# Kernel optimization log

Measured on AMD Instinct MI355X. Metric: run time of the kernel, lower is better.

## Reference

```python
import jax, jax.numpy as jnp
import numpy as np

N, E = 16384, 65536
N2, A2, E2 = 65536, 131072, 262144
N3, A3, E3 = 65536, 196608, 262144
B = 256
F_IN, NI2, NI3 = 16, 64, 64


def setup_inputs() -> dict:
    key = jax.random.key(0)
    ks = iter(jax.random.split(key, 80))
    def rn(shape, s=1.0):
        return jax.random.normal(next(ks), shape, jnp.float32) * s
    def ru(shape):
        return jax.random.uniform(next(ks), shape, dtype=jnp.float32)
    def ri(shape, hi):
        return jax.random.randint(next(ks), shape, 0, hi)
    s = 0.05
    inp = {
        "x": rn((N, F_IN)),
        "edge_index": ri((2, E), N),
        "edge_attr": ru((E, 7)),
        "batch": jnp.sort(ri((N,), B)),
        "assign2_node": ri((A2,), N),
        "assign2_cluster": ri((A2,), N2),
        "iso_type_2": ru((N2, NI2)),
        "edge_index_2": ri((2, E2), N2),
        "batch_2": jnp.sort(ri((N2,), B)),
        "assign3_node": ri((A3,), N),
        "assign3_cluster": ri((A3,), N3),
        "iso_type_3": ru((N3, NI3)),
        "edge_index_3": ri((2, E3), N3),
        "batch_3": jnp.sort(ri((N3,), B)),
    }
    for i, (mi, mo) in enumerate([(F_IN, 32), (32, 64), (64, 64)], start=1):
        inp[f"nn{i}_W1"] = rn((7, 128), s)
        inp[f"nn{i}_b1"] = jnp.zeros((128,), jnp.float32)
        inp[f"nn{i}_W2"] = rn((128, mi * mo), s)
        inp[f"nn{i}_b2"] = jnp.zeros((mi * mo,), jnp.float32)
        inp[f"conv{i}_root"] = rn((mi, mo), s)
        inp[f"conv{i}_bias"] = jnp.zeros((mo,), jnp.float32)
    for i, din in zip([4, 5, 6, 7], [64 + NI2, 64, 64 + NI3, 64]):
        inp[f"conv{i}_Wrel"] = rn((din, 64), s)
        inp[f"conv{i}_Wroot"] = rn((din, 64), s)
        inp[f"conv{i}_bias"] = jnp.zeros((64,), jnp.float32)
    inp["fc1_W"] = rn((384, 64), s); inp["fc1_b"] = jnp.zeros((64,), jnp.float32)
    inp["fc2_W"] = rn((64, 32), s); inp["fc2_b"] = jnp.zeros((32,), jnp.float32)
    inp["fc3_W"] = rn((32, 1), s); inp["fc3_b"] = jnp.zeros((1,), jnp.float32)
    return inp


def nnconv(x, ei, ea, W1, b1, W2, b2, root, bias, mi, mo):
    # edge MLP -> per-edge [mi, mo] weight matrix; message = x_src @ W_e; scatter-add to dst
    h = jax.nn.relu(ea @ W1 + b1) @ W2 + b2          # [E, mi*mo]
    We = h.reshape(-1, mi, mo)
    msg = jnp.einsum('ei,eio->eo', x[ei[0]], We)     # [E, mo]
    agg = jax.ops.segment_sum(msg, ei[1], num_segments=x.shape[0])
    return x @ root + agg + bias


def graphconv(x, ei, Wrel, Wroot, bias):
    agg = jax.ops.segment_sum(x[ei[0]], ei[1], num_segments=x.shape[0])
    return agg @ Wrel + x @ Wroot + bias


def avg_pool_assign(x, node_idx, cluster_idx, num_clusters):
    s = jax.ops.segment_sum(x[node_idx], cluster_idx, num_segments=num_clusters)
    c = jax.ops.segment_sum(jnp.ones((node_idx.shape[0],), x.dtype), cluster_idx, num_segments=num_clusters)
    return s / jnp.clip(c, 1.0)[:, None]


def reference(x, edge_index, edge_attr, batch, assign2_node, assign2_cluster, iso_type_2, edge_index_2, batch_2, assign3_node, assign3_cluster, iso_type_3, edge_index_3, batch_3, nn1_W1, nn1_b1, nn1_W2, nn1_b2, conv1_root, conv1_bias, nn2_W1, nn2_b1, nn2_W2, nn2_b2, conv2_root, conv2_bias, nn3_W1, nn3_b1, nn3_W2, nn3_b2, conv3_root, conv3_bias, conv4_Wrel, conv4_Wroot, conv4_bias, conv5_Wrel, conv5_Wroot, conv5_bias, conv6_Wrel, conv6_Wroot, conv6_bias, conv7_Wrel, conv7_Wroot, conv7_bias, fc1_W, fc1_b, fc2_W, fc2_b, fc3_W, fc3_b):
    elu = jax.nn.elu
    h = elu(nnconv(x, edge_index, edge_attr, nn1_W1, nn1_b1, nn1_W2, nn1_b2, conv1_root, conv1_bias, F_IN, 32))
    h = elu(nnconv(h, edge_index, edge_attr, nn2_W1, nn2_b1, nn2_W2, nn2_b2, conv2_root, conv2_bias, 32, 64))
    h = elu(nnconv(h, edge_index, edge_attr, nn3_W1, nn3_b1, nn3_W2, nn3_b2, conv3_root, conv3_bias, 64, 64))
    x_1 = jax.ops.segment_sum(h, batch, num_segments=B)
    # 2-set level
    h2 = avg_pool_assign(h, assign2_node, assign2_cluster, N2)
    h2 = jnp.concatenate([h2, iso_type_2], axis=1)
    h2 = elu(graphconv(h2, edge_index_2, conv4_Wrel, conv4_Wroot, conv4_bias))
    h2 = elu(graphconv(h2, edge_index_2, conv5_Wrel, conv5_Wroot, conv5_bias))
    x_2 = jax.ops.segment_sum(h2, batch_2, num_segments=B)
    # 3-set level
    h3 = avg_pool_assign(h, assign3_node, assign3_cluster, N3)
    h3 = jnp.concatenate([h3, iso_type_3], axis=1)
    h3 = elu(graphconv(h3, edge_index_3, conv6_Wrel, conv6_Wroot, conv6_bias))
    h3 = elu(graphconv(h3, edge_index_3, conv7_Wrel, conv7_Wroot, conv7_bias))
    x_3 = jax.ops.segment_sum(h3, batch_3, num_segments=B)
    xc = jnp.concatenate([x_1, x_2, x_3], axis=1)
    xc = jnp.concatenate([xc, xc], axis=1)      # [B, 384]
    o = elu(xc @ fc1_W + fc1_b)
    o = elu(o @ fc2_W + fc2_b)
    o = o @ fc3_W + fc3_b
    return o.reshape(-1)
```

## Files before the change

kernel.cpp:

```cpp
#include <hip/hip_runtime.h>
#include <math.h>

#define NN 16384
#define E1N 65536
#define NBATCH 256
#define NC2 65536
#define KH 128
#define MNSTR 1092
#define OCS 136
#define ECAP 96

typedef _Float16 f16;
typedef _Float16 f16x2 __attribute__((ext_vector_type(2)));
typedef _Float16 f16x4 __attribute__((ext_vector_type(4)));
typedef _Float16 f16x8 __attribute__((ext_vector_type(8)));
typedef float    f32x4 __attribute__((ext_vector_type(4)));

__device__ __forceinline__ float elu1(float x){ return x > 0.f ? x : expm1f(x); }

__device__ __forceinline__ float dot2acc(f16x2 a, f16x2 b, float c){
#if __has_builtin(__builtin_amdgcn_fdot2)
  return __builtin_amdgcn_fdot2(a, b, c, false);
#else
  return fmaf((float)a[0], (float)b[0], fmaf((float)a[1], (float)b[1], c));
#endif
}

__global__ __launch_bounds__(256) void k_count(const int* __restrict__ arr, int* __restrict__ cnt, int n){
  int i = blockIdx.x*256 + threadIdx.x;
  if (i < n) atomicAdd(&cnt[arr[i]], 1);
}

__global__ __launch_bounds__(256) void k_scan1(const int* __restrict__ deg,
    int* __restrict__ ptr, int* __restrict__ partials){
  __shared__ int buf[256];
  int i = blockIdx.x*256 + threadIdx.x, t = threadIdx.x;
  int v = deg[i];
  buf[t] = v; __syncthreads();
  for (int o = 1; o < 256; o <<= 1){
    int x = (t >= o) ? buf[t-o] : 0;
    __syncthreads(); buf[t] += x; __syncthreads();
  }
  ptr[i] = buf[t] - v;
  if (t == 255) partials[blockIdx.x] = buf[255];
}

__global__ __launch_bounds__(256) void k_scan2(int* __restrict__ partials, int nb){
  __shared__ int buf[256];
  int t = threadIdx.x;
  int v = (t < nb) ? partials[t] : 0;
  buf[t] = v; __syncthreads();
  for (int o = 1; o < 256; o <<= 1){
    int x = (t >= o) ? buf[t-o] : 0;
    __syncthreads(); buf[t] += x; __syncthreads();
  }
  if (t < nb) partials[t] = buf[t] - v;
}

__global__ __launch_bounds__(256) void k_scan3(const int* __restrict__ partials,
    int* __restrict__ ptr, int* __restrict__ cur){
  int i = blockIdx.x*256 + threadIdx.x;
  int v = ptr[i] + partials[blockIdx.x];
  ptr[i] = v; cur[i] = v;
}

__global__ __launch_bounds__(256) void k_fill_edge(const int* __restrict__ ei, int* __restrict__ cursor,
    int* __restrict__ eids, int* __restrict__ srcs, int* __restrict__ dsts){
  int e = blockIdx.x*256 + threadIdx.x;
  if (e >= E1N) return;
  int s = ei[e];
  int p = atomicAdd(&cursor[s], 1);
  eids[p] = e; srcs[p] = s; dsts[p] = ei[E1N + e];
}

__global__ __launch_bounds__(256) void k_fill_dst(const int* __restrict__ eiL, int* __restrict__ cur,
    int* __restrict__ dsrc, int EL){
  int e = blockIdx.x*256 + threadIdx.x;
  if (e >= EL) return;
  int d = eiL[EL + e];
  int p = atomicAdd(&cur[d], 1);
  dsrc[p] = eiL[e];
}

__global__ __launch_bounds__(256) void k_fill_assign(const int* __restrict__ an, const int* __restrict__ ac,
    int* __restrict__ cur, int* __restrict__ an_sorted, int A){
  int a = blockIdx.x*256 + threadIdx.x;
  if (a >= A) return;
  int c = ac[a];
  int p = atomicAdd(&cur[c], 1);
  an_sorted[p] = an[a];
}

__global__ __launch_bounds__(256) void k_cvt16(const float* __restrict__ v, f16* __restrict__ o, int n){
  int t = blockIdx.x*256 + threadIdx.x;
  if (t < n) o[t] = (f16)v[t];
}

__global__ __launch_bounds__(256) void k_elu_both(float* __restrict__ v, f16* __restrict__ v16, int n){
  int t = blockIdx.x*256 + threadIdx.x;
  if (t < n){ float r = elu1(v[t]); v[t] = r; v16[t] = (f16)r; }
}

__global__ __launch_bounds__(256) void k_elu(float* __restrict__ v, int n){
  int t = blockIdx.x*256 + threadIdx.x;
  if (t < n) v[t] = elu1(v[t]);
}

__global__ __launch_bounds__(256) void k_packPrep(const float* __restrict__ root,
    const float* __restrict__ b2, f16* __restrict__ Bp, int mi, int mo, int S, int NB){
  int t = blockIdx.x*256 + threadIdx.x;
  if (t >= NB*S*512) return;
  int j = t & 7, l = (t >> 3) & 63, cs = t >> 9;
  int s = cs % S, c = cs / S;
  int k_in = s*32 + ((l>>4)<<3) + j;
  int n = c*16 + (l & 15);
  float v = 0.f;
  if (k_in < mi) v = (n < mo) ? root[k_in*mo + n] : b2[k_in*mo + (n - mo)];
  Bp[t] = (f16)v;
}

template<int MI, int S, int NB, int MO>
__global__ __launch_bounds__(256) void k_prep_mfma(const f16* __restrict__ A,
    const f16* __restrict__ Bp, const float* __restrict__ bias,
    float* __restrict__ outb, float* __restrict__ bterm){
  int l = threadIdx.x & 63, w = threadIdx.x >> 6;
  int r0 = blockIdx.x*64 + w*16;
  const f16* arow = A + (size_t)(r0 + (l & 15))*MI;
  f16x8 a[S];
  #pragma unroll
  for (int s=0;s<S;s++){
    int koff = s*32 + ((l>>4)<<3);
    if (koff < MI) a[s] = *(const f16x8*)(arow + koff);
    else           a[s] = (f16x8){0,0,0,0,0,0,0,0};
  }
  #pragma unroll
  for (int c=0;c<NB;c++){
    f32x4 acc = (f32x4){0.f,0.f,0.f,0.f};
    #pragma unroll
    for (int s=0;s<S;s++){
      f16x8 b = *(const f16x8*)(Bp + ((size_t)(c*S + s)*64 + l)*8);
      acc = __builtin_amdgcn_mfma_f32_16x16x32_f16(a[s], b, acc, 0, 0, 0);
    }
    int col = c*16 + (l & 15);
    #pragma unroll
    for (int r=0;r<4;r++){
      int row = r0 + ((l>>4)<<2) + r;
      if (col < MO) outb[(size_t)row*MO + col] = acc[r] + bias[col];
      else          bterm[(size_t)row*MO + (col - MO)] = acc[r];
    }
  }
}

__global__ __launch_bounds__(256) void k_w2pack_full(const float* __restrict__ W2,
    f16* __restrict__ Bp, int mi, int mo, int S){
  int t = blockIdx.x*256 + threadIdx.x;
  if (t >= mo*8*S*512) return;
  int j = t & 7, l = (t >> 3) & 63, cs = t >> 9;
  int s = cs % S, q = cs / S;
  int oc = q >> 3;
  int k  = (q & 7)*16 + (l & 15);
  int i  = s*32 + ((l>>4)<<3) + j;
  float v = (i < mi) ? W2[(size_t)k*mi*mo + (size_t)i*mo + oc] : 0.f;
  Bp[t] = (f16)v;
}

template<int MI, int S, int MO>
__global__ __launch_bounds__(256) void k_nnconv_fused3(const f16* __restrict__ xin16,
    const f16* __restrict__ W2p,
    const int* __restrict__ rowptr, const int* __restrict__ rowend,
    const int* __restrict__ srcs, const int* __restrict__ dsts,
    const int* __restrict__ eids,
    const float* __restrict__ ea, const float* __restrict__ W1,
    const float* __restrict__ b1,
    const float* __restrict__ bterm, float* __restrict__ outb){
  __shared__ __align__(16) f16   M[16*MNSTR];
  __shared__ __align__(16) f16   hb[ECAP*OCS];
  __shared__ __align__(16) float eas[ECAP*8];
  int t = threadIdx.x, l = t & 63, w = t >> 6;
  int n0 = blockIdx.x*16;
  int estart = rowptr[n0], eend = rowend[n0+15];
  if (estart >= eend) return;
  const f16* arow = xin16 + (size_t)(n0 + (l&15))*MI;
  f16x8 a[S];
  #pragma unroll
  for (int s=0;s<S;s++){
    int koff = s*32 + ((l>>4)<<3);
    if (koff < MI) a[s] = *(const f16x8*)(arow + koff);
    else           a[s] = (f16x8){0,0,0,0,0,0,0,0};
  }
  const int NCHUNK = MO/8;
  int oc = t & 7, eslot = t >> 3;
  for (int ebase = estart; ebase < eend; ebase += ECAP){
    int ecnt = eend - ebase; if (ecnt > ECAP) ecnt = ECAP;
    for (int idx = t; idx < ecnt*8; idx += 256){
      int e_ = idx >> 3, i = idx & 7;
      eas[idx] = (i < 7) ? ea[(size_t)eids[ebase + e_]*7 + i] : 0.f;
    }
    __syncthreads();
    for (int idx = t; idx < ecnt*32; idx += 256){
      int e_ = idx >> 5, p = idx & 31;
      int k0 = p*4;
      const float* xr = &eas[e_*8];
      float4 acc4 = *(const float4*)(b1 + k0);
      #pragma unroll
      for (int i=0;i<7;i++){
        float xv = xr[i];
        float4 wv = *(const float4*)(W1 + i*KH + k0);
        acc4.x = fmaf(xv, wv.x, acc4.x);
        acc4.y = fmaf(xv, wv.y, acc4.y);
        acc4.z = fmaf(xv, wv.z, acc4.z);
        acc4.w = fmaf(xv, wv.w, acc4.w);
      }
      f16x4 hv = { (f16)fmaxf(acc4.x,0.f), (f16)fmaxf(acc4.y,0.f),
                   (f16)fmaxf(acc4.z,0.f), (f16)fmaxf(acc4.w,0.f) };
      *(f16x4*)&hb[e_*OCS + k0] = hv;
    }
    __syncthreads();
    for (int c = 0; c < NCHUNK; c++){
      #pragma unroll
      for (int tt = 0; tt < 16; tt++){
        int q = c*64 + w*16 + tt;
        f32x4 acc = (f32x4){0.f,0.f,0.f,0.f};
        #pragma unroll
        for (int s=0;s<S;s++){
          f16x8 b = *(const f16x8*)(W2p + ((size_t)(q*S + s)*64 + l)*8);
          acc = __builtin_amdgcn_mfma_f32_16x16x32_f16(a[s], b, acc, 0, 0, 0);
        }
        int ocl = w*2 + (tt>>3);
        int kpos = (tt&7)*16 + (l & 15);
        f16* mp = &M[ocl*OCS + kpos];
        #pragma unroll
        for (int r=0;r<4;r++)
          mp[(size_t)(((l>>4)<<2) + r)*MNSTR] = (f16)acc[r];
      }
      __syncthreads();
      #pragma unroll
      for (int r2 = 0; r2 < ECAP/32; r2++){
        int ee = r2*32 + eslot;
        if (ee < ecnt){
          int e = ebase + ee;
          int s_ = srcs[e];
          int ln = s_ - n0;
          float acc = bterm[(size_t)s_*MO + c*8 + oc];
          const f16* mrow = &M[(size_t)ln*MNSTR + oc*OCS];
          const f16* hrow = &hb[ee*OCS];
          #pragma unroll 4
          for (int kk=0; kk<16; kk++){
            f16x8 h8 = *(const f16x8*)(hrow + kk*8);
            f16x4 m0 = *(const f16x4*)(mrow + kk*8);
            f16x4 m1 = *(const f16x4*)(mrow + kk*8 + 4);
            acc = dot2acc((f16x2){h8[0],h8[1]}, (f16x2){m0[0],m0[1]}, acc);
            acc = dot2acc((f16x2){h8[2],h8[3]}, (f16x2){m0[2],m0[3]}, acc);
            acc = dot2acc((f16x2){h8[4],h8[5]}, (f16x2){m1[0],m1[1]}, acc);
            acc = dot2acc((f16x2){h8[6],h8[7]}, (f16x2){m1[2],m1[3]}, acc);
          }
          atomicAdd(&outb[(size_t)dsts[e]*MO + c*8 + oc], acc);
        }
      }
      __syncthreads();
    }
  }
}

__global__ __launch_bounds__(256) void k_pool_gather(const int* __restrict__ aptr,
    const int* __restrict__ aend, const int* __restrict__ an_sorted,
    const float* __restrict__ h, const float* __restrict__ iso,
    f16* __restrict__ h16){
  int l = threadIdx.x & 63, w = threadIdx.x >> 6;
  int c = blockIdx.x*4 + w;
  int st = aptr[c], en = aend[c];
  float acc = 0.f;
  int e = st;
  for (; e+1 < en; e += 2){
    int n0 = an_sorted[e], n1 = an_sorted[e+1];
    acc += h[(size_t)n0*64 + l];
    acc += h[(size_t)n1*64 + l];
  }
  if (e < en) acc += h[(size_t)an_sorted[e]*64 + l];
  int cnt = en - st;
  float val = (cnt > 0) ? acc / (float)cnt : 0.f;
  h16[(size_t)c*128 + l] = (f16)val;
  h16[(size_t)c*128 + 64 + l] = (f16)iso[(size_t)c*64 + l];
}

__global__ __launch_bounds__(256) void k_packB_gc(const float* __restrict__ Wrel,
    const float* __restrict__ Wroot, f16* __restrict__ Bp, int S){
  int t = blockIdx.x*256 + threadIdx.x;
  if (t >= 8*S*512) return;
  int j = t & 7, l = (t >> 3) & 63, cs = t >> 9;
  int s = cs % S, c = cs / S;
  int k = s*32 + ((l>>4)<<3) + j;
  int n = (c<<4) + (l & 15);
  float v = (n < 64) ? Wrel[k*64 + n] : Wroot[k*64 + (n - 64)];
  Bp[t] = (f16)v;
}

template<int S>
__global__ __launch_bounds__(256) void k_gc_mfma(const f16* __restrict__ A,
    const f16* __restrict__ Bp, const float* __restrict__ bias,
    float* __restrict__ y, float* __restrict__ rbuf){
  int l = threadIdx.x & 63, w = threadIdx.x >> 6;
  int r0 = blockIdx.x*64 + w*16;
  const f16* arow = A + (size_t)(r0 + (l & 15))*(S*32);
  f16x8 a[S];
  #pragma unroll
  for (int s=0;s<S;s++) a[s] = *(const f16x8*)(arow + s*32 + ((l>>4)<<3));
  f32x4 acc[8];
  #pragma unroll
  for (int c=0;c<8;c++) acc[c] = (f32x4){0.f,0.f,0.f,0.f};
  #pragma unroll
  for (int c=0;c<8;c++){
    #pragma unroll
    for (int s=0;s<S;s++){
      f16x8 b = *(const f16x8*)(Bp + ((size_t)(c*S + s)*64 + l)*8);
      acc[c] = __builtin_amdgcn_mfma_f32_16x16x32_f16(a[s], b, acc[c], 0, 0, 0);
    }
  }
  #pragma unroll
  for (int c=0;c<8;c++){
    int col = c*16 + (l & 15);
    #pragma unroll
    for (int r=0;r<4;r++){
      int row = r0 + ((l>>4)<<2) + r;
      if (col < 64) y[(size_t)row*64 + col] = acc[c][r];
      else          rbuf[(size_t)row*64 + (col-64)] = acc[c][r] + bias[col-64];
    }
  }
}

template<bool F16OUT>
__global__ __launch_bounds__(256) void k_gc_gather(const int* __restrict__ dptr,
    const int* __restrict__ dend, const int* __restrict__ dsrc,
    const float* __restrict__ y, const float* __restrict__ rbuf,
    f16* __restrict__ o16, float* __restrict__ o32){
  int l = threadIdx.x & 63, w = threadIdx.x >> 6;
  int n = blockIdx.x*4 + w;
  int st = dptr[n], en = dend[n];
  float acc = rbuf[(size_t)n*64 + l];
  int e = st;
  for (; e+1 < en; e += 2){
    int s0 = dsrc[e], s1 = dsrc[e+1];
    acc += y[(size_t)s0*64 + l];
    acc += y[(size_t)s1*64 + l];
  }
  if (e < en) acc += y[(size_t)dsrc[e]*64 + l];
  float r = elu1(acc);
  if (F16OUT) o16[(size_t)n*64 + l] = (f16)r;
  else        o32[(size_t)n*64 + l] = r;
}

__device__ __forceinline__ int lowerb(const int* __restrict__ a, int n, int key){
  int lo = 0, hi = n;
  while (lo < hi){ int m = (lo + hi) >> 1; if (a[m] < key) lo = m + 1; else hi = m; }
  return lo;
}

__global__ __launch_bounds__(256) void k_batchsum_seg(const int* __restrict__ batch,
    const float* __restrict__ h, float* __restrict__ x123, int n_nodes, int off){
  __shared__ float red[4][64];
  int b = blockIdx.x;
  int lo = lowerb(batch, n_nodes, b);
  int hi = lowerb(batch, n_nodes, b+1);
  int col = threadIdx.x & 63, wq = threadIdx.x >> 6;
  float acc = 0.f;
  for (int n = lo + wq; n < hi; n += 4) acc += h[(size_t)n*64 + col];
  red[wq][col] = acc;
  __syncthreads();
  if (threadIdx.x < 64){
    float s = red[0][threadIdx.x] + red[1][threadIdx.x] + red[2][threadIdx.x] + red[3][threadIdx.x];
    x123[b*192 + off + threadIdx.x] = s;
  }
}

__global__ __launch_bounds__(256) void k_fc1(const float* __restrict__ x123,
    const float* __restrict__ W, const float* __restrict__ b, float* __restrict__ t1){
  int t = blockIdx.x*256 + threadIdx.x;
  if (t >= NBATCH*64) return;
  int bb = t >> 6, o = t & 63;
  const float* xr = x123 + bb*192;
  float acc = b[o];
  for (int j=0;j<192;j++) acc = fmaf(xr[j], W[j*64+o] + W[(192+j)*64+o], acc);
  t1[t] = elu1(acc);
}

__global__ __launch_bounds__(256) void k_fc2(const float* __restrict__ t1,
    const float* __restrict__ W, const float* __restrict__ b, float* __restrict__ t2){
  int t = blockIdx.x*256 + threadIdx.x;
  if (t >= NBATCH*32) return;
  int bb = t >> 5, o = t & 31;
  float acc = b[o];
  for (int j=0;j<64;j++) acc = fmaf(t1[bb*64+j], W[j*32+o], acc);
  t2[t] = elu1(acc);
}

__global__ __launch_bounds__(256) void k_fc3(const float* __restrict__ t2,
    const float* __restrict__ W, const float* __restrict__ b, float* __restrict__ out){
  int t = blockIdx.x*256 + threadIdx.x;
  if (t >= NBATCH) return;
  float acc = b[0];
  for (int j=0;j<32;j++) acc = fmaf(t2[t*32+j], W[j], acc);
  out[t] = acc;
}

static inline int cdiv(long long a, int b){ return (int)((a + b - 1) / b); }

extern "C" void kernel_launch(void* const* d_in, const int* in_sizes, int n_in,
                              void* d_out, int out_size, void* d_ws, size_t ws_size,
                              hipStream_t stream) {
  const float* x0    = (const float*)d_in[0];
  const int*   ei    = (const int*)d_in[1];
  const float* ea    = (const float*)d_in[2];
  const int*   batch = (const int*)d_in[3];
  const int*   a2n   = (const int*)d_in[4];
  const int*   a2c   = (const int*)d_in[5];
  const float* iso2  = (const float*)d_in[6];
  const int*   ei2   = (const int*)d_in[7];
  const int*   b2arr = (const int*)d_in[8];
  const int*   a3n   = (const int*)d_in[9];
  const int*   a3c   = (const int*)d_in[10];
  const float* iso3  = (const float*)d_in[11];
  const int*   ei3   = (const int*)d_in[12];
  const int*   b3arr = (const int*)d_in[13];
  const float* nnp[3][6];
  for (int c=0;c<3;c++) for (int p=0;p<6;p++) nnp[c][p] = (const float*)d_in[14 + 6*c + p];
  const float* c4W[3]; const float* c5W[3]; const float* c6W[3]; const float* c7W[3];
  for (int p=0;p<3;p++){ c4W[p]=(const float*)d_in[32+p]; c5W[p]=(const float*)d_in[35+p];
                         c6W[p]=(const float*)d_in[38+p]; c7W[p]=(const float*)d_in[41+p]; }
  const float* fc1W=(const float*)d_in[44]; const float* fc1b=(const float*)d_in[45];
  const float* fc2W=(const float*)d_in[46]; const float* fc2b=(const float*)d_in[47];
  const float* fc3W=(const float*)d_in[48]; const float* fc3b=(const float*)d_in[49];
  float* outp = (float*)d_out;

  char* ws = (char*)d_ws; size_t off = 0;
  auto alloc = [&](size_t bytes)->void*{ void* p = ws + off; off += (bytes + 255) & ~(size_t)255; return p; };
  const size_t SZ_R0 = (size_t)92*1024*1024;
  char* r0 = (char*)alloc(SZ_R0);
  f16*   W2p   = (f16*)r0;
  f16*   prepB = (f16*)(r0 + 2*1024*1024);
  float* bterm = (float*)(r0 + 2*1024*1024 + 64*1024);
  size_t o2 = 0;
  auto a2 = [&](size_t bytes)->char*{ char* p = r0 + o2; o2 += (bytes + 255) & ~(size_t)255; return p; };
  f16*   h16   = (f16*)  a2((size_t)NC2*128*2);
  float* ybuf  = (float*)a2((size_t)NC2*64*4);
  float* rbuf  = (float*)a2((size_t)NC2*64*4);
  float* gB    = (float*)a2((size_t)NC2*64*4);
  f16*   g16   = (f16*)  a2((size_t)NC2*64*2);
  f16*   BpGc  = (f16*)  a2((size_t)8*4*512*2);
  int*   aptr  = (int*)  a2((size_t)NC2*4);
  int*   acur  = (int*)  a2((size_t)NC2*4);
  int*   dptr  = (int*)  a2((size_t)NC2*4);
  int*   dcur  = (int*)  a2((size_t)NC2*4);
  int*   ldeg  = (int*)  a2((size_t)NC2*4);
  int*   ans   = (int*)  a2((size_t)196608*4);
  int*   dsrc  = (int*)  a2((size_t)262144*4);
  float* hA    = (float*)alloc((size_t)NN*32*4);
  float* hB    = (float*)alloc((size_t)NN*64*4);
  float* hC    = (float*)alloc((size_t)NN*64*4);
  f16*   x016  = (f16*)  alloc((size_t)NN*16*2);
  f16*   hA16  = (f16*)  alloc((size_t)NN*32*2);
  f16*   hB16  = (f16*)  alloc((size_t)NN*64*2);
  int*   deg   = (int*)  alloc((size_t)NN*4);
  int*   cursor= (int*)  alloc((size_t)NN*4);
  int*   rowptr= (int*)  alloc((size_t)NN*4);
  int*   eids  = (int*)  alloc((size_t)E1N*4);
  int*   srcs  = (int*)  alloc((size_t)E1N*4);
  int*   dsts  = (int*)  alloc((size_t)E1N*4);
  int*   parts = (int*)  alloc((size_t)256*4);
  float* x123  = (float*)alloc((size_t)NBATCH*192*4);
  float* t1    = (float*)alloc((size_t)NBATCH*64*4);
  float* t2    = (float*)alloc((size_t)NBATCH*32*4);
  (void)ws_size; (void)n_in; (void)in_sizes; (void)out_size;

  auto scan = [&](const int* dg, int n, int* ptr, int* cur){
    k_scan1<<<n/256,256,0,stream>>>(dg, ptr, parts);
    k_scan2<<<1,256,0,stream>>>(parts, n/256);
    k_scan3<<<n/256,256,0,stream>>>(parts, ptr, cur);
  };

  hipMemsetAsync(deg, 0, (size_t)NN*4, stream);
  k_count<<<cdiv(E1N,256),256,0,stream>>>(ei, deg, E1N);
  scan(deg, NN, rowptr, cursor);
  k_fill_edge<<<cdiv(E1N,256),256,0,stream>>>(ei, cursor, eids, srcs, dsts);
  k_cvt16<<<cdiv((long long)NN*16,256),256,0,stream>>>(x0, x016, NN*16);

  auto run_nnconv = [&](const f16* xin16, int mi, int mo,
                        const float* const* P, float* outb, f16* out16){
    const float* W1=P[0]; const float* b1=P[1]; const float* W2=P[2];
    const float* b2=P[3]; const float* root=P[4]; const float* bias=P[5];
    const int S = (mi > 32) ? 2 : 1;
    const int NB = (2*mo)/16;
    k_packPrep<<<cdiv((long long)NB*S*512,256),256,0,stream>>>(root, b2, prepB, mi, mo, S, NB);
    if (mi==16)      k_prep_mfma<16,1,4,32><<<NN/64,256,0,stream>>>(xin16, prepB, bias, outb, bterm);
    else if (mi==32) k_prep_mfma<32,1,8,64><<<NN/64,256,0,stream>>>(xin16, prepB, bias, outb, bterm);
    else             k_prep_mfma<64,2,8,64><<<NN/64,256,0,stream>>>(xin16, prepB, bias, outb, bterm);
    k_w2pack_full<<<cdiv((long long)mo*8*S*512,256),256,0,stream>>>(W2, W2p, mi, mo, S);
    if (mi==16)      k_nnconv_fused3<16,1,32><<<NN/16,256,0,stream>>>(xin16, W2p, rowptr, cursor, srcs, dsts, eids, ea, W1, b1, bterm, outb);
    else if (mi==32) k_nnconv_fused3<32,1,64><<<NN/16,256,0,stream>>>(xin16, W2p, rowptr, cursor, srcs, dsts, eids, ea, W1, b1, bterm, outb);
    else             k_nnconv_fused3<64,2,64><<<NN/16,256,0,stream>>>(xin16, W2p, rowptr, cursor, srcs, dsts, eids, ea, W1, b1, bterm, outb);
    if (out16) k_elu_both<<<cdiv((long long)NN*mo,256),256,0,stream>>>(outb, out16, NN*mo);
    else       k_elu<<<cdiv((long long)NN*mo,256),256,0,stream>>>(outb, NN*mo);
  };
  run_nnconv(x016, 16, 32, nnp[0], hA, hA16);
  run_nnconv(hA16, 32, 64, nnp[1], hB, hB16);
  run_nnconv(hB16, 64, 64, nnp[2], hC, nullptr);

  k_batchsum_seg<<<NBATCH,256,0,stream>>>(batch, hC, x123, NN, 0);

  auto run_level = [&](const int* an, const int* ac, int A, const float* iso,
                       const int* eiL, int EL, const int* batchL,
                       const float* const* cA, const float* const* cB, int off123){
    hipMemsetAsync(ldeg, 0, (size_t)NC2*4, stream);
    k_count<<<cdiv(A,256),256,0,stream>>>(ac, ldeg, A);
    scan(ldeg, NC2, aptr, acur);
    k_fill_assign<<<cdiv(A,256),256,0,stream>>>(an, ac, acur, ans, A);
    hipMemsetAsync(ldeg, 0, (size_t)NC2*4, stream);
    k_count<<<cdiv(EL,256),256,0,stream>>>(eiL + EL, ldeg, EL);
    scan(ldeg, NC2, dptr, dcur);
    k_fill_dst<<<cdiv(EL,256),256,0,stream>>>(eiL, dcur, dsrc, EL);
    k_pool_gather<<<NC2/4,256,0,stream>>>(aptr, acur, ans, hC, iso, h16);
    k_packB_gc<<<cdiv((long long)8*4*512,256),256,0,stream>>>(cA[0], cA[1], BpGc, 4);
    k_gc_mfma<4><<<NC2/64,256,0,stream>>>(h16, BpGc, cA[2], ybuf, rbuf);
    k_gc_gather<true><<<NC2/4,256,0,stream>>>(dptr, dcur, dsrc, ybuf, rbuf, g16, nullptr);
    k_packB_gc<<<cdiv((long long)8*2*512,256),256,0,stream>>>(cB[0], cB[1], BpGc, 2);
    k_gc_mfma<2><<<NC2/64,256,0,stream>>>(g16, BpGc, cB[2], ybuf, rbuf);
    k_gc_gather<false><<<NC2/4,256,0,stream>>>(dptr, dcur, dsrc, ybuf, rbuf, nullptr, gB);
    k_batchsum_seg<<<NBATCH,256,0,stream>>>(batchL, gB, x123, NC2, off123);
  };
  run_level(a2n, a2c, 131072, iso2, ei2, 262144, b2arr, c4W, c5W, 64);
  run_level(a3n, a3c, 196608, iso3, ei3, 262144, b3arr, c6W, c7W, 128);

  k_fc1<<<cdiv((long long)NBATCH*64,256),256,0,stream>>>(x123, fc1W, fc1b, t1);
  k_fc2<<<cdiv((long long)NBATCH*32,256),256,0,stream>>>(t1, fc2W, fc2b, t2);
  k_fc3<<<cdiv(NBATCH,256),256,0,stream>>>(t2, fc3W, fc3b, outp);
}
```

Measured before the change: 868.3 us.

## Halve nnconv output-chunk width and move set-level intermediates to fp16

The fused NNConv kernel now builds the per-node edge-weight slab for 4 output channels per chunk instead of 8. This halves its shared-memory tile stride and lets more edges be processed per pass, at the cost of twice as many chunks and barriers. The 2-set and 3-set levels now store hC, the GraphConv outputs, root terms and final gather results as fp16 instead of fp32, which halves gather and scan memory traffic at some cost in precision. The standalone fp32-only ELU kernel is dropped, so the last NNConv layer also writes an fp16 copy.

```diff
diff --git a/kernel.cpp b/kernel.cpp
--- a/kernel.cpp
+++ b/kernel.cpp
@@ -6,8 +6,8 @@
 #define NBATCH 256
 #define NC2 65536
 #define KH 128
-#define MNSTR 1092
 #define OCS 136
+#define MNSTR 548
 #define ECAP 96
 
 typedef _Float16 f16;
@@ -101,11 +101,6 @@
   if (t < n){ float r = elu1(v[t]); v[t] = r; v16[t] = (f16)r; }
 }
 
-__global__ __launch_bounds__(256) void k_elu(float* __restrict__ v, int n){
-  int t = blockIdx.x*256 + threadIdx.x;
-  if (t < n) v[t] = elu1(v[t]);
-}
-
 __global__ __launch_bounds__(256) void k_packPrep(const float* __restrict__ root,
     const float* __restrict__ b2, f16* __restrict__ Bp, int mi, int mo, int S, int NB){
   int t = blockIdx.x*256 + threadIdx.x;
@@ -165,7 +160,7 @@
 }
 
 template<int MI, int S, int MO>
-__global__ __launch_bounds__(256) void k_nnconv_fused3(const f16* __restrict__ xin16,
+__global__ __launch_bounds__(256) void k_nnconv_fused4(const f16* __restrict__ xin16,
     const f16* __restrict__ W2p,
     const int* __restrict__ rowptr, const int* __restrict__ rowend,
     const int* __restrict__ srcs, const int* __restrict__ dsts,
@@ -188,8 +183,8 @@
     if (koff < MI) a[s] = *(const f16x8*)(arow + koff);
     else           a[s] = (f16x8){0,0,0,0,0,0,0,0};
   }
-  const int NCHUNK = MO/8;
-  int oc = t & 7, eslot = t >> 3;
+  const int NCHUNK = MO/4;
+  int oc = t & 3, eslot = t >> 2;
   for (int ebase = estart; ebase < eend; ebase += ECAP){
     int ecnt = eend - ebase; if (ecnt > ECAP) ecnt = ECAP;
     for (int idx = t; idx < ecnt*8; idx += 256){
@@ -218,30 +213,29 @@
     __syncthreads();
     for (int c = 0; c < NCHUNK; c++){
       #pragma unroll
-      for (int tt = 0; tt < 16; tt++){
-        int q = c*64 + w*16 + tt;
+      for (int tt = 0; tt < 8; tt++){
+        int q = (c*4 + w)*8 + tt;
         f32x4 acc = (f32x4){0.f,0.f,0.f,0.f};
         #pragma unroll
         for (int s=0;s<S;s++){
           f16x8 b = *(const f16x8*)(W2p + ((size_t)(q*S + s)*64 + l)*8);
           acc = __builtin_amdgcn_mfma_f32_16x16x32_f16(a[s], b, acc, 0, 0, 0);
         }
-        int ocl = w*2 + (tt>>3);
-        int kpos = (tt&7)*16 + (l & 15);
-        f16* mp = &M[ocl*OCS + kpos];
+        int kpos = tt*16 + (l & 15);
+        f16* mp = &M[w*OCS + kpos];
         #pragma unroll
         for (int r=0;r<4;r++)
           mp[(size_t)(((l>>4)<<2) + r)*MNSTR] = (f16)acc[r];
       }
       __syncthreads();
       #pragma unroll
-      for (int r2 = 0; r2 < ECAP/32; r2++){
-        int ee = r2*32 + eslot;
+      for (int r2 = 0; r2 < ECAP/48; r2++){
+        int ee = r2*64 + eslot;
         if (ee < ecnt){
           int e = ebase + ee;
           int s_ = srcs[e];
           int ln = s_ - n0;
-          float acc = bterm[(size_t)s_*MO + c*8 + oc];
+          float acc = bterm[(size_t)s_*MO + c*4 + oc];
           const f16* mrow = &M[(size_t)ln*MNSTR + oc*OCS];
           const f16* hrow = &hb[ee*OCS];
           #pragma unroll 4
@@ -254,7 +248,7 @@
             acc = dot2acc((f16x2){h8[4],h8[5]}, (f16x2){m1[0],m1[1]}, acc);
             acc = dot2acc((f16x2){h8[6],h8[7]}, (f16x2){m1[2],m1[3]}, acc);
           }
-          atomicAdd(&outb[(size_t)dsts[e]*MO + c*8 + oc], acc);
+          atomicAdd(&outb[(size_t)dsts[e]*MO + c*4 + oc], acc);
         }
       }
       __syncthreads();
@@ -264,7 +258,7 @@
 
 __global__ __launch_bounds__(256) void k_pool_gather(const int* __restrict__ aptr,
     const int* __restrict__ aend, const int* __restrict__ an_sorted,
-    const float* __restrict__ h, const float* __restrict__ iso,
+    const f16* __restrict__ h, const float* __restrict__ iso,
     f16* __restrict__ h16){
   int l = threadIdx.x & 63, w = threadIdx.x >> 6;
   int c = blockIdx.x*4 + w;
@@ -273,10 +267,10 @@
   int e = st;
   for (; e+1 < en; e += 2){
     int n0 = an_sorted[e], n1 = an_sorted[e+1];
-    acc += h[(size_t)n0*64 + l];
-    acc += h[(size_t)n1*64 + l];
-  }
-  if (e < en) acc += h[(size_t)an_sorted[e]*64 + l];
+    acc += (float)h[(size_t)n0*64 + l];
+    acc += (float)h[(size_t)n1*64 + l];
+  }
+  if (e < en) acc += (float)h[(size_t)an_sorted[e]*64 + l];
   int cnt = en - st;
   float val = (cnt > 0) ? acc / (float)cnt : 0.f;
   h16[(size_t)c*128 + l] = (f16)val;
@@ -298,7 +292,7 @@
 template<int S>
 __global__ __launch_bounds__(256) void k_gc_mfma(const f16* __restrict__ A,
     const f16* __restrict__ Bp, const float* __restrict__ bias,
-    float* __restrict__ y, float* __restrict__ rbuf){
+    f16* __restrict__ y16, f16* __restrict__ rbuf16){
   int l = threadIdx.x & 63, w = threadIdx.x >> 6;
   int r0 = blockIdx.x*64 + w*16;
   const f16* arow = A + (size_t)(r0 + (l & 15))*(S*32);
@@ -322,31 +316,28 @@
     #pragma unroll
     for (int r=0;r<4;r++){
       int row = r0 + ((l>>4)<<2) + r;
-      if (col < 64) y[(size_t)row*64 + col] = acc[c][r];
-      else          rbuf[(size_t)row*64 + (col-64)] = acc[c][r] + bias[col-64];
-    }
-  }
-}
-
-template<bool F16OUT>
+      if (col < 64) y16[(size_t)row*64 + col] = (f16)acc[c][r];
+      else          rbuf16[(size_t)row*64 + (col-64)] = (f16)(acc[c][r] + bias[col-64]);
+    }
+  }
+}
+
 __global__ __launch_bounds__(256) void k_gc_gather(const int* __restrict__ dptr,
     const int* __restrict__ dend, const int* __restrict__ dsrc,
-    const float* __restrict__ y, const float* __restrict__ rbuf,
-    f16* __restrict__ o16, float* __restrict__ o32){
+    const f16* __restrict__ y16, const f16* __restrict__ rbuf16,
+    f16* __restrict__ o16){
   int l = threadIdx.x & 63, w = threadIdx.x >> 6;
   int n = blockIdx.x*4 + w;
   int st = dptr[n], en = dend[n];
-  float acc = rbuf[(size_t)n*64 + l];
+  float acc = (float)rbuf16[(size_t)n*64 + l];
   int e = st;
   for (; e+1 < en; e += 2){
     int s0 = dsrc[e], s1 = dsrc[e+1];
-    acc += y[(size_t)s0*64 + l];
-    acc += y[(size_t)s1*64 + l];
-  }
-  if (e < en) acc += y[(size_t)dsrc[e]*64 + l];
-  float r = elu1(acc);
-  if (F16OUT) o16[(size_t)n*64 + l] = (f16)r;
-  else        o32[(size_t)n*64 + l] = r;
+    acc += (float)y16[(size_t)s0*64 + l];
+    acc += (float)y16[(size_t)s1*64 + l];
+  }
+  if (e < en) acc += (float)y16[(size_t)dsrc[e]*64 + l];
+  o16[(size_t)n*64 + l] = (f16)elu1(acc);
 }
 
 __device__ __forceinline__ int lowerb(const int* __restrict__ a, int n, int key){
@@ -355,15 +346,18 @@
   return lo;
 }
 
+template<bool F16IN>
 __global__ __launch_bounds__(256) void k_batchsum_seg(const int* __restrict__ batch,
-    const float* __restrict__ h, float* __restrict__ x123, int n_nodes, int off){
+    const float* __restrict__ h32, const f16* __restrict__ h16,
+    float* __restrict__ x123, int n_nodes, int off){
   __shared__ float red[4][64];
   int b = blockIdx.x;
   int lo = lowerb(batch, n_nodes, b);
   int hi = lowerb(batch, n_nodes, b+1);
   int col = threadIdx.x & 63, wq = threadIdx.x >> 6;
   float acc = 0.f;
-  for (int n = lo + wq; n < hi; n += 4) acc += h[(size_t)n*64 + col];
+  for (int n = lo + wq; n < hi; n += 4)
+    acc += F16IN ? (float)h16[(size_t)n*64 + col] : h32[(size_t)n*64 + col];
   red[wq][col] = acc;
   __syncthreads();
   if (threadIdx.x < 64){
@@ -441,9 +435,9 @@
   size_t o2 = 0;
   auto a2 = [&](size_t bytes)->char*{ char* p = r0 + o2; o2 += (bytes + 255) & ~(size_t)255; return p; };
   f16*   h16   = (f16*)  a2((size_t)NC2*128*2);
-  float* ybuf  = (float*)a2((size_t)NC2*64*4);
-  float* rbuf  = (float*)a2((size_t)NC2*64*4);
-  float* gB    = (float*)a2((size_t)NC2*64*4);
+  f16*   y16   = (f16*)  a2((size_t)NC2*64*2);
+  f16*   rbuf16= (f16*)  a2((size_t)NC2*64*2);
+  f16*   gB16  = (f16*)  a2((size_t)NC2*64*2);
   f16*   g16   = (f16*)  a2((size_t)NC2*64*2);
   f16*   BpGc  = (f16*)  a2((size_t)8*4*512*2);
   int*   aptr  = (int*)  a2((size_t)NC2*4);
@@ -459,6 +453,7 @@
   f16*   x016  = (f16*)  alloc((size_t)NN*16*2);
   f16*   hA16  = (f16*)  alloc((size_t)NN*32*2);
   f16*   hB16  = (f16*)  alloc((size_t)NN*64*2);
+  f16*   hC16  = (f16*)  alloc((size_t)NN*64*2);
   int*   deg   = (int*)  alloc((size_t)NN*4);
   int*   cursor= (int*)  alloc((size_t)NN*4);
   int*   rowptr= (int*)  alloc((size_t)NN*4);
@@ -494,17 +489,16 @@
     else if (mi==32) k_prep_mfma<32,1,8,64><<<NN/64,256,0,stream>>>(xin16, prepB, bias, outb, bterm);
     else             k_prep_mfma<64,2,8,64><<<NN/64,256,0,stream>>>(xin16, prepB, bias, outb, bterm);
     k_w2pack_full<<<cdiv((long long)mo*8*S*512,256),256,0,stream>>>(W2, W2p, mi, mo, S);
-    if (mi==16)      k_nnconv_fused3<16,1,32><<<NN/16,256,0,stream>>>(xin16, W2p, rowptr, cursor, srcs, dsts, eids, ea, W1, b1, bterm, outb);
-    else if (mi==32) k_nnconv_fused3<32,1,64><<<NN/16,256,0,stream>>>(xin16, W2p, rowptr, cursor, srcs, dsts, eids, ea, W1, b1, bterm, outb);
-    else             k_nnconv_fused3<64,2,64><<<NN/16,256,0,stream>>>(xin16, W2p, rowptr, cursor, srcs, dsts, eids, ea, W1, b1, bterm, outb);
-    if (out16) k_elu_both<<<cdiv((long long)NN*mo,256),256,0,stream>>>(outb, out16, NN*mo);
-    else       k_elu<<<cdiv((long long)NN*mo,256),256,0,stream>>>(outb, NN*mo);
+    if (mi==16)      k_nnconv_fused4<16,1,32><<<NN/16,256,0,stream>>>(xin16, W2p, rowptr, cursor, srcs, dsts, eids, ea, W1, b1, bterm, outb);
+    else if (mi==32) k_nnconv_fused4<32,1,64><<<NN/16,256,0,stream>>>(xin16, W2p, rowptr, cursor, srcs, dsts, eids, ea, W1, b1, bterm, outb);
+    else             k_nnconv_fused4<64,2,64><<<NN/16,256,0,stream>>>(xin16, W2p, rowptr, cursor, srcs, dsts, eids, ea, W1, b1, bterm, outb);
+    k_elu_both<<<cdiv((long long)NN*mo,256),256,0,stream>>>(outb, out16, NN*mo);
   };
   run_nnconv(x016, 16, 32, nnp[0], hA, hA16);
   run_nnconv(hA16, 32, 64, nnp[1], hB, hB16);
-  run_nnconv(hB16, 64, 64, nnp[2], hC, nullptr);
-
-  k_batchsum_seg<<<NBATCH,256,0,stream>>>(batch, hC, x123, NN, 0);
+  run_nnconv(hB16, 64, 64, nnp[2], hC, hC16);
+
+  k_batchsum_seg<false><<<NBATCH,256,0,stream>>>(batch, hC, nullptr, x123, NN, 0);
 
   auto run_level = [&](const int* an, const int* ac, int A, const float* iso,
                        const int* eiL, int EL, const int* batchL,
@@ -517,14 +511,14 @@
     k_count<<<cdiv(EL,256),256,0,stream>>>(eiL + EL, ldeg, EL);
     scan(ldeg, NC2, dptr, dcur);
     k_fill_dst<<<cdiv(EL,256),256,0,stream>>>(eiL, dcur, dsrc, EL);
-    k_pool_gather<<<NC2/4,256,0,stream>>>(aptr, acur, ans, hC, iso, h16);
+    k_pool_gather<<<NC2/4,256,0,stream>>>(aptr, acur, ans, hC16, iso, h16);
     k_packB_gc<<<cdiv((long long)8*4*512,256),256,0,stream>>>(cA[0], cA[1], BpGc, 4);
-    k_gc_mfma<4><<<NC2/64,256,0,stream>>>(h16, BpGc, cA[2], ybuf, rbuf);
-    k_gc_gather<true><<<NC2/4,256,0,stream>>>(dptr, dcur, dsrc, ybuf, rbuf, g16, nullptr);
+    k_gc_mfma<4><<<NC2/64,256,0,stream>>>(h16, BpGc, cA[2], y16, rbuf16);
+    k_gc_gather<<<NC2/4,256,0,stream>>>(dptr, dcur, dsrc, y16, rbuf16, g16);
     k_packB_gc<<<cdiv((long long)8*2*512,256),256,0,stream>>>(cB[0], cB[1], BpGc, 2);
-    k_gc_mfma<2><<<NC2/64,256,0,stream>>>(g16, BpGc, cB[2], ybuf, rbuf);
-    k_gc_gather<false><<<NC2/4,256,0,stream>>>(dptr, dcur, dsrc, ybuf, rbuf, nullptr, gB);
-    k_batchsum_seg<<<NBATCH,256,0,stream>>>(batchL, gB, x123, NC2, off123);
+    k_gc_mfma<2><<<NC2/64,256,0,stream>>>(g16, BpGc, cB[2], y16, rbuf16);
+    k_gc_gather<<<NC2/4,256,0,stream>>>(dptr, dcur, dsrc, y16, rbuf16, gB16);
+    k_batchsum_seg<true><<<NBATCH,256,0,stream>>>(batchL, nullptr, gB16, x123, NC2, off123);
   };
   run_level(a2n, a2c, 131072, iso2, ei2, 262144, b2arr, c4W, c5W, 64);
   run_level(a3n, a3c, 196608, iso3, ei3, 262144, b3arr, c6W, c7W, 128);
```

Result: slower. 901.9 us (+3.9%).
